# Kernel optimization log

Hardware: AMD Instinct MI355X
Metric: run time of the kernel (lower is better)

Reference implementation:

```python
import jax, jax.numpy as jnp
import numpy as np

NUM_EMBEDDINGS = 8192
EMBEDDING_DIM = 256
BETA = 0.25


def setup_inputs() -> dict:
    key = jax.random.key(0)
    k1, k2 = jax.random.split(key)
    z = jax.random.normal(k1, (16, 256, 32, 32), dtype=jnp.float32)
    # torch init: uniform(-1/K, 1/K)
    emb_w = jax.random.uniform(k2, (NUM_EMBEDDINGS, EMBEDDING_DIM),
                               dtype=jnp.float32,
                               minval=-1.0 / NUM_EMBEDDINGS,
                               maxval=1.0 / NUM_EMBEDDINGS)
    return {"z": z, "emb_w": emb_w}


def reference(z, emb_w):
    B, C, H, W = z.shape
    z_bhwc = jnp.transpose(z, (0, 2, 3, 1))          # [B,H,W,C]
    flat = z_bhwc.reshape(-1, C)                      # [N,C]
    d = (jnp.sum(flat * flat, axis=1, keepdims=True)
         + jnp.sum(emb_w * emb_w, axis=1)
         - 2.0 * flat @ emb_w.T)                      # [N,K]
    idx = jnp.argmin(d, axis=1)                       # [N]
    # direct gather (mathematically identical to one-hot @ emb_w)
    quantized = emb_w[idx].reshape(z_bhwc.shape)      # [B,H,W,C]
    q_latent_loss = jnp.mean((jax.lax.stop_gradient(quantized) - z_bhwc) ** 2)
    e_latent_loss = jnp.mean((quantized - jax.lax.stop_gradient(z_bhwc)) ** 2)
    loss = q_latent_loss + BETA * e_latent_loss
    # straight-through estimator
    quantized_st = z_bhwc + jax.lax.stop_gradient(quantized - z_bhwc)
    out = jnp.transpose(quantized_st, (0, 3, 1, 2))   # [B,C,H,W]
    return out, loss, idx.reshape(B, -1)
```

## Files before the change

kernel.cpp:

```cpp
#include <hip/hip_runtime.h>
#include <cstdint>
#include <cstddef>

#define N_PIX   16384
#define K_EMB   8192
#define DDIM    256

#define WS_A8       0
#define WS_E8       4194304
#define WS_KEYS     6291456
#define WS_ZSQ      23068672
#define WS_ESQ      23134208
#define WS_LOSS     23166976
#define WS_CNT      23166984

typedef float f32x16 __attribute__((ext_vector_type(16)));
typedef int   i32x4  __attribute__((ext_vector_type(4)));
typedef int   i32x8  __attribute__((ext_vector_type(8)));

__device__ __forceinline__ unsigned int f32_sortable(float f) {
    unsigned int u = __float_as_uint(f);
    return (u & 0x80000000u) ? ~u : (u | 0x80000000u);
}

__device__ __forceinline__ unsigned char f2fp8(float x) {
    unsigned ub = __float_as_uint(x);
    unsigned sgn = (ub >> 24) & 0x80u;
    unsigned b = ub & 0x7FFFFFFFu;
    unsigned out;
    if (__uint_as_float(b) < 0.015625f) {
        out = (unsigned)(int)rintf(__uint_as_float(b) * 512.0f);
    } else {
        unsigned r = b + 0x7FFFFu + ((b >> 20) & 1u);
        int er = (int)(r >> 23) - 127;
        out = (unsigned)(((er + 7) << 3) | ((r >> 20) & 7u));
    }
    return (unsigned char)(out | sgn);
}

#if defined(__has_builtin)
#if __has_builtin(__builtin_amdgcn_cvt_pk_fp8_f32)
#define HAVE_CVT_FP8 1
#endif
#if __has_builtin(__builtin_amdgcn_fmed3f)
#define HAVE_FMED3 1
#endif
#endif

__device__ __forceinline__ unsigned pack4_fp8(float a, float b, float c, float d) {
#ifdef HAVE_CVT_FP8
    int pk = 0;
    pk = __builtin_amdgcn_cvt_pk_fp8_f32(a, b, pk, false);
    pk = __builtin_amdgcn_cvt_pk_fp8_f32(c, d, pk, true);
    return (unsigned)pk;
#else
    return (unsigned)f2fp8(a) | ((unsigned)f2fp8(b) << 8)
         | ((unsigned)f2fp8(c) << 16) | ((unsigned)f2fp8(d) << 24);
#endif
}

__device__ __forceinline__ void async16(const unsigned char* g, unsigned char* l) {
    __builtin_amdgcn_global_load_lds(
        (const __attribute__((address_space(1))) void*)g,
        (__attribute__((address_space(3))) void*)l, 16, 0, 0);
}

__device__ __forceinline__ float np_pairwise_sq256(const float* row) {
    float r[16];
#pragma unroll
    for (int j = 0; j < 16; ++j) r[j] = 0.f;
#pragma unroll
    for (int c = 0; c < 256; ++c) {
        float x  = row[c];
        float sq = __fmul_rn(x, x);
        int slot = ((c >> 7) << 3) | (c & 7);
        r[slot] = __fadd_rn(r[slot], sq);
    }
    float h0 = __fadd_rn(
        __fadd_rn(__fadd_rn(r[0], r[1]), __fadd_rn(r[2], r[3])),
        __fadd_rn(__fadd_rn(r[4], r[5]), __fadd_rn(r[6], r[7])));
    float h1 = __fadd_rn(
        __fadd_rn(__fadd_rn(r[8], r[9]), __fadd_rn(r[10], r[11])),
        __fadd_rn(__fadd_rn(r[12], r[13]), __fadd_rn(r[14], r[15])));
    return __fadd_rn(h0, h1);
}

__global__ __launch_bounds__(256) void prep_kernel(
        const float* __restrict__ z, const float* __restrict__ emb,
        unsigned char* __restrict__ Af8, unsigned char* __restrict__ Ef8,
        float* __restrict__ zsq, float* __restrict__ esq,
        double* __restrict__ lossAcc, unsigned* __restrict__ doneCnt) {
    __shared__ float tile[32][257];
    int blk = blockIdx.x;
    int t   = threadIdx.x;
    if (blk < 512) {
        int b   = blk >> 5;
        int hw0 = (blk & 31) * 32;
        const float* zb = z + (size_t)b * 262144 + hw0;
        int c0  = t >> 3;
        int px4 = t & 7;
#pragma unroll
        for (int cc = 0; cc < 8; ++cc) {
            int c = cc * 32 + c0;
            float4 v = *(const float4*)&zb[(size_t)c * 1024 + px4 * 4];
            tile[px4 * 4 + 0][c] = v.x;
            tile[px4 * 4 + 1][c] = v.y;
            tile[px4 * 4 + 2][c] = v.z;
            tile[px4 * 4 + 3][c] = v.w;
        }
        __syncthreads();
        int p0 = b * 1024 + hw0;
        int wv = t >> 6, lane = t & 63;
#pragma unroll
        for (int iter = 0; iter < 8; ++iter) {
            int pl = iter * 4 + wv;
            unsigned pk = pack4_fp8(tile[pl][lane * 4 + 0], tile[pl][lane * 4 + 1],
                                    tile[pl][lane * 4 + 2], tile[pl][lane * 4 + 3]);
            int p  = p0 + pl;
            int mbb = p >> 7, r = p & 127;
            int c = lane * 4;
            *(unsigned*)(Af8 + (size_t)mbb * 32768
                         + (c >> 6) * 8192 + r * 64 + (c & 63)) = pk;
        }
        if (t < 32) zsq[p0 + t] = np_pairwise_sq256(tile[t]);
        if (blk == 0 && t == 0) { *lossAcc = 0.0; *doneCnt = 0u; }
    } else {
        int k0 = (blk - 512) * 32;
        const float4* eg = (const float4*)(emb + (size_t)k0 * DDIM);
#pragma unroll
        for (int i = 0; i < 8; ++i) {
            int idx = i * 256 + t;
            int row = idx >> 6, c4 = idx & 63;
            float4 v = eg[idx];
            *(float4*)&tile[row][c4 * 4] = v;
        }
        __syncthreads();
#pragma unroll
        for (int i = 0; i < 8; ++i) {
            int idx = i * 256 + t;
            int row = idx >> 6, c4 = idx & 63;
            const float* rp = &tile[row][c4 * 4];
            int kg = k0 + row;
            int nbb = kg >> 7, rr = kg & 127;
            int c  = c4 * 4;
            int kk = c >> 6, kl = c & 63;
            int s  = kl >> 4;
            int pos = kk * 8192 + rr * 64
                    + ((s ^ ((rr >> 1) & 3)) << 4) + (kl & 15);
            *(unsigned*)(Ef8 + (size_t)nbb * 32768 + pos) =
                pack4_fp8(rp[0] * 8192.0f, rp[1] * 8192.0f,
                          rp[2] * 8192.0f, rp[3] * 8192.0f);
        }
        if (t < 32) esq[k0 + t] = np_pairwise_sq256(tile[t]);
    }
}

__device__ __forceinline__ unsigned pack_key(float w) {
    float uf = __builtin_fmaf(w, -512.0f, 262144.0f);
    uf = fminf(uf, 524287.0f);
    unsigned u = (unsigned)uf;
    return (u << 13) | (__float_as_uint(w) & 0x1FFFu);
}

__global__ __launch_bounds__(256) void mfma_score_kernel(
        const unsigned char* __restrict__ Af8,
        const unsigned char* __restrict__ Ef8,
        unsigned int* __restrict__ keys) {
    union __align__(16) SM {
        unsigned char Bs[2][32768];
        struct { uint2 ep[128][33]; } e;
    };
    __shared__ SM sm;

    const int g  = blockIdx.x;
    const int mb = blockIdx.y;
    const int t = threadIdx.x;
    const int w = t >> 6, lane = t & 63;
    const int wm = w >> 1, wn = w & 1;
    const int l31 = lane & 31, h = lane >> 5;

    {
        const unsigned char* Eg = Ef8 + (size_t)(g * 4) * 32768 + t * 16;
#pragma unroll
        for (int ch = 0; ch < 8; ++ch)
            async16(Eg + ch * 4096, &sm.Bs[0][ch * 4096 + t * 16]);
    }

    i32x8 afr[2][4];
    {
        const unsigned char* Ab = Af8 + (size_t)mb * 32768;
#pragma unroll
        for (int rt = 0; rt < 2; ++rt) {
            int r = wm * 64 + rt * 32 + l31;
#pragma unroll
            for (int kk = 0; kk < 4; ++kk) {
                const unsigned char* p = Ab + kk * 8192 + r * 64 + h * 32;
                i32x4 lo = *(const i32x4*)p;
                i32x4 hi = *(const i32x4*)(p + 16);
                afr[rt][kk] = __builtin_shufflevector(lo, hi,
                                                      0, 1, 2, 3, 4, 5, 6, 7);
            }
        }
    }

    const float NEGINF = __int_as_float(0xFF800000);
    float t2a[2][16], t2b[2][16];
#pragma unroll
    for (int rt = 0; rt < 2; ++rt)
#pragma unroll
        for (int q = 0; q < 16; ++q) { t2a[rt][q] = NEGINF; t2b[rt][q] = NEGINF; }

    __syncthreads();

#pragma unroll 1
    for (int j = 0; j < 4; ++j) {
        const int cur = j & 1, nxt = cur ^ 1;

        if (j < 3) {
            const unsigned char* Eg =
                Ef8 + (size_t)(g * 4 + j + 1) * 32768 + t * 16;
#pragma unroll
            for (int ch = 0; ch < 8; ++ch)
                async16(Eg + ch * 4096, &sm.Bs[nxt][ch * 4096 + t * 16]);
        }

        f32x16 acc[2][2];
#pragma unroll
        for (int rt = 0; rt < 2; ++rt)
#pragma unroll
            for (int ct = 0; ct < 2; ++ct)
#pragma unroll
                for (int q = 0; q < 16; ++q) acc[rt][ct][q] = 0.f;

#pragma unroll
        for (int kk = 0; kk < 4; ++kk) {
            i32x8 bf[2];
#pragma unroll
            for (int ct = 0; ct < 2; ++ct) {
                int c = wn * 64 + ct * 32 + l31;
                int m = (c >> 1) & 3;
                int base = kk * 8192 + c * 64;
                int s0 = h * 2;
                i32x4 lo = *(const i32x4*)
                    &sm.Bs[cur][base + ((s0 ^ m) << 4)];
                i32x4 hi = *(const i32x4*)
                    &sm.Bs[cur][base + (((s0 + 1) ^ m) << 4)];
                bf[ct] = __builtin_shufflevector(lo, hi,
                                                 0, 1, 2, 3, 4, 5, 6, 7);
            }
            __builtin_amdgcn_s_setprio(1);
#pragma unroll
            for (int rt = 0; rt < 2; ++rt)
#pragma unroll
                for (int ct = 0; ct < 2; ++ct)
                    acc[rt][ct] =
                        __builtin_amdgcn_mfma_scale_f32_32x32x64_f8f6f4(
                            afr[rt][kk], bf[ct], acc[rt][ct],
                            0, 0,
                            0, 0x7F7F7F7F,
                            0, 0x7F7F7F7F);
            __builtin_amdgcn_s_setprio(0);
        }

        const int nb = g * 4 + j;
#pragma unroll
        for (int ct = 0; ct < 2; ++ct) {
            const unsigned idxc = (unsigned)(nb * 128 + wn * 64 + ct * 32 + l31);
#pragma unroll
            for (int rt = 0; rt < 2; ++rt) {
#pragma unroll
                for (int q = 0; q < 16; ++q) {
                    float v = acc[rt][ct][q];
                    float wv = __uint_as_float(
                        (__float_as_uint(v) & 0xFFFFE000u) | idxc);
                    float a0 = t2a[rt][q], b0 = t2b[rt][q];
#ifdef HAVE_FMED3
                    float bn = __builtin_amdgcn_fmed3f(a0, wv, b0);
                    t2a[rt][q] = fmaxf(a0, wv);
                    t2b[rt][q] = bn;
#else
                    float mn = fminf(a0, wv);
                    t2a[rt][q] = fmaxf(a0, wv);
                    t2b[rt][q] = fmaxf(b0, mn);
#endif
                }
            }
        }
        __syncthreads();
    }

#pragma unroll
    for (int rt = 0; rt < 2; ++rt) {
#pragma unroll
        for (int q = 0; q < 16; ++q) {
            unsigned ka = pack_key(t2a[rt][q]);
            unsigned kb = pack_key(t2b[rt][q]);
            unsigned pa = (unsigned)__shfl_xor((int)ka, 16, 64);
            unsigned pb = (unsigned)__shfl_xor((int)kb, 16, 64);
            unsigned n0 = min(ka, pa);
            unsigned n1 = min(max(ka, pa), min(kb, pb));
            if ((lane & 16) == 0) {
                int row = wm * 64 + rt * 32 + (q & 3) + 8 * (q >> 2) + 4 * h;
                sm.e.ep[row][wn * 16 + (lane & 15)] = make_uint2(n0, n1);
            }
        }
    }
    __syncthreads();

    {
        int row = t >> 1, half = t & 1, h0 = half * 16;
        uint2 mv = sm.e.ep[row][h0];
#pragma unroll
        for (int i = 1; i < 16; ++i) {
            uint2 av = sm.e.ep[row][h0 + i];
            unsigned n0 = min(mv.x, av.x);
            unsigned n1 = min(max(mv.x, av.x), min(mv.y, av.y));
            mv.x = n0; mv.y = n1;
        }
        ((uint2*)keys)[(size_t)(g * 2 + half) * N_PIX + (mb * 128 + row)] = mv;
    }
}

__global__ __launch_bounds__(256) void final_kernel(
        const unsigned int* __restrict__ keys,
        const float* __restrict__ z, const float* __restrict__ emb,
        const float* __restrict__ zsq, const float* __restrict__ esq,
        float* __restrict__ out, float* __restrict__ idx_out,
        float* __restrict__ loss_out,
        double* __restrict__ lossAcc, unsigned* __restrict__ doneCnt) {
    __shared__ float ztile[16][260];
    __shared__ uint2 kt[16][33];
    __shared__ int   scand[16][64];
    __shared__ unsigned long long ckey[1024];
    __shared__ int   soff[17];
    __shared__ int   scnt[16];
    __shared__ int   pxmap[1024];
    __shared__ float szs[16];
    __shared__ int   sidx[16];

    int blk = blockIdx.x;
    int b = blk >> 6, hh = blk & 63;
    int t = threadIdx.x;
    int p0 = b * 1024 + hh * 16;
    const float* zb = z + (size_t)b * 262144 + hh * 16;
    {
        int px = t & 15, cb = t >> 4;
#pragma unroll
        for (int cc = 0; cc < 16; ++cc) {
            int c = cc * 16 + cb;
            ztile[px][c] = zb[(size_t)c * 1024 + px];
        }
    }
    {
        const uint2* kg = (const uint2*)keys;
#pragma unroll
        for (int itr = 0; itr < 2; ++itr) {
            int idx = itr * 256 + t;
            int px = idx & 15, hf = idx >> 4;
            kt[px][hf] = kg[(size_t)hf * N_PIX + p0 + px];
        }
    }
    if (t < 16) szs[t] = zsq[p0 + t];
    __syncthreads();

    {
        int wq = t >> 6, lane = t & 63;
#pragma unroll 1
        for (int i = 0; i < 4; ++i) {
            int px = wq * 4 + i;
            uint2 ka = (lane < 32) ? kt[px][lane] : make_uint2(~0u, ~0u);
            unsigned m = min(ka.x, ka.y);
#pragma unroll
            for (int off = 32; off >= 1; off >>= 1)
                m = min(m, (unsigned)__shfl_xor((int)m, off, 64));
            unsigned thr = (m >> 13) + 1600;

            bool h0 = (lane < 32) && ((ka.x >> 13) <= thr);
            bool h1 = (lane < 32) && ((ka.y >> 13) <= thr);
            unsigned long long m0 = __ballot(h0);
            unsigned long long m1 = __ballot(h1);
            int c0 = __popcll(m0);
            unsigned long long below = (lane == 63) ? ~0ull >> 1
                                     : ((1ull << lane) - 1);
            if (h0) scand[px][__popcll(m0 & below)] = (int)(ka.x & 0x1FFFu);
            if (h1) scand[px][c0 + __popcll(m1 & below)] = (int)(ka.y & 0x1FFFu);
            if (lane == 0) scnt[px] = c0 + __popcll(m1);
        }
    }
    __syncthreads();

    if (t < 64) {
        int v = (t < 16) ? scnt[t] : 0;
#pragma unroll
        for (int o = 1; o < 16; o <<= 1) {
            int u = __shfl_up(v, o, 64);
            if (t >= o) v += u;
        }
        if (t < 16) soff[t + 1] = v;
        if (t == 0) soff[0] = 0;
    }
    __syncthreads();
    int total = soff[16];
    for (int f = t; f < total; f += 256) {
        int lo = 0, hi = 15;
        while (lo < hi) {
            int mid = (lo + hi + 1) >> 1;
            if (soff[mid] <= f) lo = mid; else hi = mid - 1;
        }
        pxmap[f] = lo;
    }
    __syncthreads();

    {
        int gid = t >> 4, l16 = t & 15;
        const float4* emb4 = (const float4*)emb;
#pragma unroll 1
        for (int f = gid; f < total; f += 16) {
            int px = pxmap[f];
            int k  = scand[px][f - soff[px]];
            double d = 0.0;
#pragma unroll
            for (int q = 0; q < 4; ++q) {
                float4 ev = emb4[(size_t)k * 64 + q * 16 + l16];
                const float* zp = &ztile[px][(q * 16 + l16) * 4];
                d += (double)zp[0] * ev.x + (double)zp[1] * ev.y
                   + (double)zp[2] * ev.z + (double)zp[3] * ev.w;
            }
#pragma unroll
            for (int o = 1; o < 16; o <<= 1) d += __shfl_xor(d, o, 64);
            if (l16 == 0) {
                float df = (float)d;
                float s  = __fsub_rn(__fadd_rn(szs[px], esq[k]),
                                     __fmul_rn(2.0f, df));
                ckey[f] = ((unsigned long long)f32_sortable(s) << 32)
                        | (unsigned)k;
            }
        }
    }
    __syncthreads();

    {
        int cpx = t >> 4, ci = t & 15;
        unsigned long long best = ~0ull;
        for (int f = soff[cpx] + ci; f < soff[cpx + 1]; f += 16) {
            unsigned long long v = ckey[f];
            best = v < best ? v : best;
        }
#pragma unroll
        for (int o = 1; o < 16; o <<= 1) {
            unsigned long long ov =
                (unsigned long long)__shfl_xor((long long)best, o, 64);
            best = ov < best ? ov : best;
        }
        if (ci == 0) {
            int k = (int)(unsigned)(best & 0xffffffffu);
            sidx[cpx] = k;
            idx_out[p0 + cpx] = (float)k;
        }
    }
    __syncthreads();

    int px2 = t & 15, cy = t >> 4;
    int kk = sidx[px2];
    const float* er = emb + (size_t)kk * DDIM;
    float* ob = out + (size_t)b * 262144 + hh * 16;
    float local = 0.f;
#pragma unroll 4
    for (int it = 0; it < 16; ++it) {
        int c = it * 16 + cy;
        float q = er[c];
        float d = q - ztile[px2][c];
        ob[(size_t)c * 1024 + px2] = q;
        local += d * d;
    }
#pragma unroll
    for (int off = 32; off >= 1; off >>= 1) local += __shfl_down(local, off, 64);
    __shared__ float wsum[4];
    if ((t & 63) == 0) wsum[t >> 6] = local;
    __syncthreads();
    if (t == 0) {
        double s = (double)wsum[0] + (double)wsum[1]
                 + (double)wsum[2] + (double)wsum[3];
        atomicAdd(lossAcc, s);
        __threadfence();
        unsigned old = atomicAdd(doneCnt, 1u);
        if (old == 1023u) {
            double tot = atomicAdd(lossAcc, 0.0);
            *loss_out = (float)(tot * (1.25 / 4194304.0));
        }
    }
}

extern "C" void kernel_launch(void* const* d_in, const int* in_sizes, int n_in,
                              void* d_out, int out_size, void* d_ws, size_t ws_size,
                              hipStream_t stream) {
    const float* z   = (const float*)d_in[0];
    const float* emb = (const float*)d_in[1];
    float* out = (float*)d_out;
    char* ws = (char*)d_ws;

    unsigned char* Af8 = (unsigned char*)(ws + WS_A8);
    unsigned char* Ef8 = (unsigned char*)(ws + WS_E8);
    unsigned int* keys = (unsigned int*)(ws + WS_KEYS);
    float* zsq      = (float*)(ws + WS_ZSQ);
    float* esq      = (float*)(ws + WS_ESQ);
    double* lossAcc = (double*)(ws + WS_LOSS);
    unsigned* doneCnt = (unsigned*)(ws + WS_CNT);

    prep_kernel<<<768, 256, 0, stream>>>(z, emb, Af8, Ef8, zsq, esq,
                                         lossAcc, doneCnt);
    mfma_score_kernel<<<dim3(16, 128), 256, 0, stream>>>(Af8, Ef8, keys);
    final_kernel<<<1024, 256, 0, stream>>>(keys, z, emb, zsq, esq,
                                           out, out + 4194305, out + 4194304,
                                           lossAcc, doneCnt);
}
```

Baseline: 187.1 us.

## Parallelize squared-norm reduction and process 32 pixels per final block

The prep kernel's per-row squared-norm sum previously ran on only 32 threads serially over 256 elements. All 256 threads now compute partial sums into shared memory while keeping the same summation order, and 32 threads finish the tree. The final kernel now handles 32 pixels per block instead of 16, halving the grid, loading z with float4 coalesced reads and packing candidate indices into shorts and bytes to fit the larger tiles in LDS. This adds a barrier in prep and raises LDS use and per-block work in final, which may reduce occupancy.

```diff
diff --git a/kernel.cpp b/kernel.cpp
--- a/kernel.cpp
+++ b/kernel.cpp
@@ -65,32 +65,13 @@
         (__attribute__((address_space(3))) void*)l, 16, 0, 0);
 }
 
-__device__ __forceinline__ float np_pairwise_sq256(const float* row) {
-    float r[16];
-#pragma unroll
-    for (int j = 0; j < 16; ++j) r[j] = 0.f;
-#pragma unroll
-    for (int c = 0; c < 256; ++c) {
-        float x  = row[c];
-        float sq = __fmul_rn(x, x);
-        int slot = ((c >> 7) << 3) | (c & 7);
-        r[slot] = __fadd_rn(r[slot], sq);
-    }
-    float h0 = __fadd_rn(
-        __fadd_rn(__fadd_rn(r[0], r[1]), __fadd_rn(r[2], r[3])),
-        __fadd_rn(__fadd_rn(r[4], r[5]), __fadd_rn(r[6], r[7])));
-    float h1 = __fadd_rn(
-        __fadd_rn(__fadd_rn(r[8], r[9]), __fadd_rn(r[10], r[11])),
-        __fadd_rn(__fadd_rn(r[12], r[13]), __fadd_rn(r[14], r[15])));
-    return __fadd_rn(h0, h1);
-}
-
 __global__ __launch_bounds__(256) void prep_kernel(
         const float* __restrict__ z, const float* __restrict__ emb,
         unsigned char* __restrict__ Af8, unsigned char* __restrict__ Ef8,
         float* __restrict__ zsq, float* __restrict__ esq,
         double* __restrict__ lossAcc, unsigned* __restrict__ doneCnt) {
     __shared__ float tile[32][257];
+    __shared__ float sqs[32][17];
     int blk = blockIdx.x;
     int t   = threadIdx.x;
     if (blk < 512) {
@@ -122,7 +103,34 @@
             *(unsigned*)(Af8 + (size_t)mbb * 32768
                          + (c >> 6) * 8192 + r * 64 + (c & 63)) = pk;
         }
-        if (t < 32) zsq[p0 + t] = np_pairwise_sq256(tile[t]);
+        {
+            int row = t >> 3, s0 = t & 7;
+            const float* rp = tile[row];
+            float a0 = 0.f, a1 = 0.f;
+#pragma unroll
+            for (int i = 0; i < 16; ++i) {
+                float x0 = rp[s0 + 8 * i];
+                a0 = __fadd_rn(a0, __fmul_rn(x0, x0));
+            }
+#pragma unroll
+            for (int i = 0; i < 16; ++i) {
+                float x1 = rp[128 + s0 + 8 * i];
+                a1 = __fadd_rn(a1, __fmul_rn(x1, x1));
+            }
+            sqs[row][s0]     = a0;
+            sqs[row][s0 + 8] = a1;
+        }
+        __syncthreads();
+        if (t < 32) {
+            const float* r = sqs[t];
+            float h0 = __fadd_rn(
+                __fadd_rn(__fadd_rn(r[0], r[1]), __fadd_rn(r[2], r[3])),
+                __fadd_rn(__fadd_rn(r[4], r[5]), __fadd_rn(r[6], r[7])));
+            float h1 = __fadd_rn(
+                __fadd_rn(__fadd_rn(r[8], r[9]), __fadd_rn(r[10], r[11])),
+                __fadd_rn(__fadd_rn(r[12], r[13]), __fadd_rn(r[14], r[15])));
+            zsq[p0 + t] = __fadd_rn(h0, h1);
+        }
         if (blk == 0 && t == 0) { *lossAcc = 0.0; *doneCnt = 0u; }
     } else {
         int k0 = (blk - 512) * 32;
@@ -151,7 +159,34 @@
                 pack4_fp8(rp[0] * 8192.0f, rp[1] * 8192.0f,
                           rp[2] * 8192.0f, rp[3] * 8192.0f);
         }
-        if (t < 32) esq[k0 + t] = np_pairwise_sq256(tile[t]);
+        {
+            int row = t >> 3, s0 = t & 7;
+            const float* rp = tile[row];
+            float a0 = 0.f, a1 = 0.f;
+#pragma unroll
+            for (int i = 0; i < 16; ++i) {
+                float x0 = rp[s0 + 8 * i];
+                a0 = __fadd_rn(a0, __fmul_rn(x0, x0));
+            }
+#pragma unroll
+            for (int i = 0; i < 16; ++i) {
+                float x1 = rp[128 + s0 + 8 * i];
+                a1 = __fadd_rn(a1, __fmul_rn(x1, x1));
+            }
+            sqs[row][s0]     = a0;
+            sqs[row][s0 + 8] = a1;
+        }
+        __syncthreads();
+        if (t < 32) {
+            const float* r = sqs[t];
+            float h0 = __fadd_rn(
+                __fadd_rn(__fadd_rn(r[0], r[1]), __fadd_rn(r[2], r[3])),
+                __fadd_rn(__fadd_rn(r[4], r[5]), __fadd_rn(r[6], r[7])));
+            float h1 = __fadd_rn(
+                __fadd_rn(__fadd_rn(r[8], r[9]), __fadd_rn(r[10], r[11])),
+                __fadd_rn(__fadd_rn(r[12], r[13]), __fadd_rn(r[14], r[15])));
+            esq[k0 + t] = __fadd_rn(h0, h1);
+        }
     }
 }
 
@@ -328,46 +363,50 @@
         float* __restrict__ out, float* __restrict__ idx_out,
         float* __restrict__ loss_out,
         double* __restrict__ lossAcc, unsigned* __restrict__ doneCnt) {
-    __shared__ float ztile[16][260];
-    __shared__ uint2 kt[16][33];
-    __shared__ int   scand[16][64];
-    __shared__ unsigned long long ckey[1024];
-    __shared__ int   soff[17];
-    __shared__ int   scnt[16];
-    __shared__ int   pxmap[1024];
-    __shared__ float szs[16];
-    __shared__ int   sidx[16];
+    __shared__ float ztile[32][257];
+    __shared__ uint2 kt[32][33];
+    __shared__ unsigned short scand[32][64];
+    __shared__ unsigned long long ckey[2048];
+    __shared__ int   soff[33];
+    __shared__ int   scnt[32];
+    __shared__ unsigned char pxmap[2048];
+    __shared__ float szs[32];
+    __shared__ int   sidx[32];
 
     int blk = blockIdx.x;
-    int b = blk >> 6, hh = blk & 63;
+    int b = blk >> 5, hh2 = blk & 31;
     int t = threadIdx.x;
-    int p0 = b * 1024 + hh * 16;
-    const float* zb = z + (size_t)b * 262144 + hh * 16;
-    {
-        int px = t & 15, cb = t >> 4;
-#pragma unroll
-        for (int cc = 0; cc < 16; ++cc) {
-            int c = cc * 16 + cb;
-            ztile[px][c] = zb[(size_t)c * 1024 + px];
+    int p0 = b * 1024 + hh2 * 32;
+    const float* zb = z + (size_t)b * 262144 + hh2 * 32;
+    {
+        int c0 = t >> 3, px4 = t & 7;
+#pragma unroll
+        for (int cc = 0; cc < 8; ++cc) {
+            int c = cc * 32 + c0;
+            float4 v = *(const float4*)&zb[(size_t)c * 1024 + px4 * 4];
+            ztile[px4 * 4 + 0][c] = v.x;
+            ztile[px4 * 4 + 1][c] = v.y;
+            ztile[px4 * 4 + 2][c] = v.z;
+            ztile[px4 * 4 + 3][c] = v.w;
         }
     }
     {
         const uint2* kg = (const uint2*)keys;
 #pragma unroll
-        for (int itr = 0; itr < 2; ++itr) {
+        for (int itr = 0; itr < 4; ++itr) {
             int idx = itr * 256 + t;
-            int px = idx & 15, hf = idx >> 4;
+            int px = idx & 31, hf = idx >> 5;
             kt[px][hf] = kg[(size_t)hf * N_PIX + p0 + px];
         }
     }
-    if (t < 16) szs[t] = zsq[p0 + t];
+    if (t < 32) szs[t] = zsq[p0 + t];
     __syncthreads();
 
     {
         int wq = t >> 6, lane = t & 63;
 #pragma unroll 1
-        for (int i = 0; i < 4; ++i) {
-            int px = wq * 4 + i;
+        for (int i = 0; i < 8; ++i) {
+            int px = wq * 8 + i;
             uint2 ka = (lane < 32) ? kt[px][lane] : make_uint2(~0u, ~0u);
             unsigned m = min(ka.x, ka.y);
 #pragma unroll
@@ -382,32 +421,34 @@
             int c0 = __popcll(m0);
             unsigned long long below = (lane == 63) ? ~0ull >> 1
                                      : ((1ull << lane) - 1);
-            if (h0) scand[px][__popcll(m0 & below)] = (int)(ka.x & 0x1FFFu);
-            if (h1) scand[px][c0 + __popcll(m1 & below)] = (int)(ka.y & 0x1FFFu);
+            if (h0) scand[px][__popcll(m0 & below)] =
+                (unsigned short)(ka.x & 0x1FFFu);
+            if (h1) scand[px][c0 + __popcll(m1 & below)] =
+                (unsigned short)(ka.y & 0x1FFFu);
             if (lane == 0) scnt[px] = c0 + __popcll(m1);
         }
     }
     __syncthreads();
 
     if (t < 64) {
-        int v = (t < 16) ? scnt[t] : 0;
-#pragma unroll
-        for (int o = 1; o < 16; o <<= 1) {
+        int v = (t < 32) ? scnt[t] : 0;
+#pragma unroll
+        for (int o = 1; o < 32; o <<= 1) {
             int u = __shfl_up(v, o, 64);
             if (t >= o) v += u;
         }
-        if (t < 16) soff[t + 1] = v;
+        if (t < 32) soff[t + 1] = v;
         if (t == 0) soff[0] = 0;
     }
     __syncthreads();
-    int total = soff[16];
+    int total = soff[32];
     for (int f = t; f < total; f += 256) {
-        int lo = 0, hi = 15;
+        int lo = 0, hi = 31;
         while (lo < hi) {
             int mid = (lo + hi + 1) >> 1;
             if (soff[mid] <= f) lo = mid; else hi = mid - 1;
         }
-        pxmap[f] = lo;
+        pxmap[f] = (unsigned char)lo;
     }
     __syncthreads();
 
@@ -440,34 +481,38 @@
     __syncthreads();
 
     {
-        int cpx = t >> 4, ci = t & 15;
-        unsigned long long best = ~0ull;
-        for (int f = soff[cpx] + ci; f < soff[cpx + 1]; f += 16) {
-            unsigned long long v = ckey[f];
-            best = v < best ? v : best;
-        }
-#pragma unroll
-        for (int o = 1; o < 16; o <<= 1) {
-            unsigned long long ov =
-                (unsigned long long)__shfl_xor((long long)best, o, 64);
-            best = ov < best ? ov : best;
-        }
-        if (ci == 0) {
-            int k = (int)(unsigned)(best & 0xffffffffu);
-            sidx[cpx] = k;
-            idx_out[p0 + cpx] = (float)k;
-        }
-    }
-    __syncthreads();
-
-    int px2 = t & 15, cy = t >> 4;
+        int ci = t & 15;
+#pragma unroll
+        for (int pass = 0; pass < 2; ++pass) {
+            int cpx = (t >> 4) + pass * 16;
+            unsigned long long best = ~0ull;
+            for (int f = soff[cpx] + ci; f < soff[cpx + 1]; f += 16) {
+                unsigned long long v = ckey[f];
+                best = v < best ? v : best;
+            }
+#pragma unroll
+            for (int o = 1; o < 16; o <<= 1) {
+                unsigned long long ov =
+                    (unsigned long long)__shfl_xor((long long)best, o, 64);
+                best = ov < best ? ov : best;
+            }
+            if (ci == 0) {
+                int k = (int)(unsigned)(best & 0xffffffffu);
+                sidx[cpx] = k;
+                idx_out[p0 + cpx] = (float)k;
+            }
+        }
+    }
+    __syncthreads();
+
+    int px2 = t & 31, cy = t >> 5;
     int kk = sidx[px2];
     const float* er = emb + (size_t)kk * DDIM;
-    float* ob = out + (size_t)b * 262144 + hh * 16;
+    float* ob = out + (size_t)b * 262144 + hh2 * 32;
     float local = 0.f;
 #pragma unroll 4
-    for (int it = 0; it < 16; ++it) {
-        int c = it * 16 + cy;
+    for (int it = 0; it < 32; ++it) {
+        int c = it * 8 + cy;
         float q = er[c];
         float d = q - ztile[px2][c];
         ob[(size_t)c * 1024 + px2] = q;
@@ -484,7 +529,7 @@
         atomicAdd(lossAcc, s);
         __threadfence();
         unsigned old = atomicAdd(doneCnt, 1u);
-        if (old == 1023u) {
+        if (old == 511u) {
             double tot = atomicAdd(lossAcc, 0.0);
             *loss_out = (float)(tot * (1.25 / 4194304.0));
         }
@@ -510,7 +555,7 @@
     prep_kernel<<<768, 256, 0, stream>>>(z, emb, Af8, Ef8, zsq, esq,
                                          lossAcc, doneCnt);
     mfma_score_kernel<<<dim3(16, 128), 256, 0, stream>>>(Af8, Ef8, keys);
-    final_kernel<<<1024, 256, 0, stream>>>(keys, z, emb, zsq, esq,
-                                           out, out + 4194305, out + 4194304,
-                                           lossAcc, doneCnt);
-}
+    final_kernel<<<512, 256, 0, stream>>>(keys, z, emb, zsq, esq,
+                                          out, out + 4194305, out + 4194304,
+                                          lossAcc, doneCnt);
+}
```

After: 170.3 us. 9.0% less time.
